# Kernel tuning notes

Measured on AMD Instinct MI355X. Metric: run time of the kernel, lower is better.

The kernel has to match this reference:

```python
import jax, jax.numpy as jnp
import numpy as np

N_NODES = 100000
N_EDGES = 1600000
NUM_FEATURES = 128
HIDDEN = 64
NUM_CLASSES = 2


def _gcn_norm(edge_index, num_nodes):
    # PyG gcn_norm: add self-loops, symmetric degree normalization.
    loop = jnp.arange(num_nodes, dtype=edge_index.dtype)
    src = jnp.concatenate([edge_index[0], loop])
    dst = jnp.concatenate([edge_index[1], loop])
    deg = jax.ops.segment_sum(jnp.ones_like(src, dtype=jnp.float32), dst,
                              num_segments=num_nodes)
    dinv = jnp.where(deg > 0, jax.lax.rsqrt(deg), 0.0)
    norm = dinv[src] * dinv[dst]  # [E + N]
    return src, dst, norm


def _gcn_conv(x, src, dst, norm, W, b, num_nodes):
    h = x @ W  # linear transform first (PyG GCNConv)
    msg = h[src] * norm[:, None]  # gather + edge scaling, [E+N, H]
    out = jax.ops.segment_sum(msg, dst, num_segments=num_nodes)  # scatter-add
    return out + b


def setup_inputs() -> dict:
    key = jax.random.key(0)
    ks = jax.random.split(key, 8)
    x = jax.random.normal(ks[0], (N_NODES, NUM_FEATURES), dtype=jnp.float32)
    edge_index = jax.random.randint(ks[1], (2, N_EDGES), 0, N_NODES, dtype=jnp.int32)
    def glorot(k, shape):
        lim = np.sqrt(6.0 / (shape[0] + shape[1]))
        return jax.random.uniform(k, shape, jnp.float32, -lim, lim)
    return {
        "x": x,
        "edge_index": edge_index,
        "W1": glorot(ks[2], (NUM_FEATURES, HIDDEN)),
        "b1": jnp.zeros((HIDDEN,), jnp.float32),
        "W2": glorot(ks[3], (HIDDEN, HIDDEN)),
        "b2": jnp.zeros((HIDDEN,), jnp.float32),
        "W3": glorot(ks[4], (HIDDEN, HIDDEN)),
        "b3": jnp.zeros((HIDDEN,), jnp.float32),
        "Wlin": glorot(ks[5], (HIDDEN, NUM_CLASSES)),
        "blin": jnp.zeros((NUM_CLASSES,), jnp.float32),
    }


def reference(x, edge_index, W1, b1, W2, b2, W3, b3, Wlin, blin):
    num_nodes = x.shape[0]
    src, dst, norm = _gcn_norm(edge_index, num_nodes)
    # eval mode: dropout is identity
    h = jax.nn.relu(_gcn_conv(x, src, dst, norm, W1, b1, num_nodes))
    h = jax.nn.relu(_gcn_conv(h, src, dst, norm, W2, b2, num_nodes))
    h = jax.nn.relu(_gcn_conv(h, src, dst, norm, W3, b3, num_nodes))
    logits = h @ Wlin + blin
    return jax.nn.log_softmax(logits, axis=1)
```

## Files before the change

kernel.cpp:

```cpp
#include <hip/hip_runtime.h>
#include <cstdint>
#include <cstddef>

#define NF 128
#define NH 64


__global__ __launch_bounds__(256) void count_kernel(const int* __restrict__ ei, int E,
                                                    int* __restrict__ cnt) {
  int i = blockIdx.x * 256 + threadIdx.x;
  if (i * 4 >= E) return;
  int4 d = ((const int4*)(ei + E))[i];
  atomicAdd(&cnt[d.x], 1);
  atomicAdd(&cnt[d.y], 1);
  atomicAdd(&cnt[d.z], 1);
  atomicAdd(&cnt[d.w], 1);
}

__global__ __launch_bounds__(256) void partial_kernel(const int* __restrict__ cnt, int N,
                                                      int* __restrict__ part) {
  __shared__ int sd[256];
  int t = threadIdx.x;
  int idx = blockIdx.x * 1024 + t * 4;
  int s = 0;
#pragma unroll
  for (int j = 0; j < 4; ++j)
    if (idx + j < N) s += cnt[idx + j];
  sd[t] = s;
  __syncthreads();
  for (int off = 128; off > 0; off >>= 1) {
    if (t < off) sd[t] += sd[t + off];
    __syncthreads();
  }
  if (t == 0) part[blockIdx.x] = sd[0];
}

__global__ __launch_bounds__(128) void scanp_kernel(int* __restrict__ part, int NB,
                                                    int* __restrict__ rowptrN) {
  __shared__ int s[128];
  int t = threadIdx.x;
  int v = (t < NB) ? part[t] : 0;
  s[t] = v;
  __syncthreads();
  for (int off = 1; off < 128; off <<= 1) {
    int add = (t >= off) ? s[t - off] : 0;
    __syncthreads();
    s[t] += add;
    __syncthreads();
  }
  if (t < NB) part[t] = s[t] - v;
  if (t == 0) rowptrN[0] = s[127];
}

__global__ __launch_bounds__(256) void rowptr_kernel(const int* __restrict__ cnt,
                                                     const int* __restrict__ part,
                                                     int* __restrict__ rowptr,
                                                     int* __restrict__ cnt2,
                                                     float* __restrict__ dinv, int N) {
  __shared__ int s[256];
  int t = threadIdx.x;
  int idx = blockIdx.x * 1024 + t * 4;
  int c[4];
  int ts = 0;
#pragma unroll
  for (int j = 0; j < 4; ++j) {
    c[j] = (idx + j < N) ? cnt[idx + j] : 0;
    ts += c[j];
  }
  s[t] = ts;
  __syncthreads();
  for (int off = 1; off < 256; off <<= 1) {
    int add = (t >= off) ? s[t - off] : 0;
    __syncthreads();
    s[t] += add;
    __syncthreads();
  }
  int run = s[t] - ts + part[blockIdx.x];
#pragma unroll
  for (int j = 0; j < 4; ++j) {
    if (idx + j < N) {
      rowptr[idx + j] = run;
      cnt2[idx + j] = run;
      dinv[idx + j] = rsqrtf((float)(c[j] + 1));
    }
    run += c[j];
  }
}

__global__ __launch_bounds__(256) void fill_kernel(const int* __restrict__ ei, int E,
                                                   int* __restrict__ cnt2,
                                                   const float* __restrict__ dinv,
                                                   int2* __restrict__ col2,
                                                   int lo, int hi) {
  int i = blockIdx.x * 256 + threadIdx.x;
  if (i * 4 >= E) return;
  int4 sv = ((const int4*)ei)[i];
  int4 dv = ((const int4*)(ei + E))[i];
  int ss[4] = {sv.x, sv.y, sv.z, sv.w};
  int dd[4] = {dv.x, dv.y, dv.z, dv.w};
#pragma unroll
  for (int j = 0; j < 4; ++j) {
    int d = dd[j];
    if (d < lo || d >= hi) continue;
    int s = ss[j];
    float w = dinv[s] * dinv[d];
    int pos = atomicAdd(&cnt2[d], 1);
    col2[pos] = make_int2(s, __float_as_int(w));
  }
}


template <int K>
__global__ __launch_bounds__(256, 4) void gemm_kernel(const float* __restrict__ X,
                                                      const float* __restrict__ W,
                                                      float* __restrict__ H, int N) {
  __shared__ float XsT[64][68];
  __shared__ float Ws[64 * 64];
  const int tid = threadIdx.x;
  const int n0 = blockIdx.x * 64;
  const int tn = (tid >> 4) * 4;
  const int tf = (tid & 15) * 4;

  float acc[4][4];
#pragma unroll
  for (int i = 0; i < 4; ++i)
#pragma unroll
    for (int j = 0; j < 4; ++j) acc[i][j] = 0.f;

  for (int kt = 0; kt < K / 64; ++kt) {
    {
      const float4* Wg = (const float4*)(W + (size_t)kt * 64 * 64);
      float4* Wl = (float4*)Ws;
#pragma unroll
      for (int j = 0; j < 4; ++j) Wl[tid + j * 256] = Wg[tid + j * 256];
    }
#pragma unroll
    for (int j = 0; j < 4; ++j) {
      int idx = tid + j * 256;
      int n = idx >> 4;
      int kq = idx & 15;
      float4 v = make_float4(0.f, 0.f, 0.f, 0.f);
      if (n0 + n < N)
        v = *(const float4*)(X + (size_t)(n0 + n) * K + kt * 64 + kq * 4);
      XsT[kq * 4 + 0][n] = v.x;
      XsT[kq * 4 + 1][n] = v.y;
      XsT[kq * 4 + 2][n] = v.z;
      XsT[kq * 4 + 3][n] = v.w;
    }
    __syncthreads();
#pragma unroll 8
    for (int k = 0; k < 64; ++k) {
      float4 xv = *(const float4*)(&XsT[k][tn]);
      float4 wv = *(const float4*)(&Ws[k * 64 + tf]);
      acc[0][0] = fmaf(xv.x, wv.x, acc[0][0]);
      acc[0][1] = fmaf(xv.x, wv.y, acc[0][1]);
      acc[0][2] = fmaf(xv.x, wv.z, acc[0][2]);
      acc[0][3] = fmaf(xv.x, wv.w, acc[0][3]);
      acc[1][0] = fmaf(xv.y, wv.x, acc[1][0]);
      acc[1][1] = fmaf(xv.y, wv.y, acc[1][1]);
      acc[1][2] = fmaf(xv.y, wv.z, acc[1][2]);
      acc[1][3] = fmaf(xv.y, wv.w, acc[1][3]);
      acc[2][0] = fmaf(xv.z, wv.x, acc[2][0]);
      acc[2][1] = fmaf(xv.z, wv.y, acc[2][1]);
      acc[2][2] = fmaf(xv.z, wv.z, acc[2][2]);
      acc[2][3] = fmaf(xv.z, wv.w, acc[2][3]);
      acc[3][0] = fmaf(xv.w, wv.x, acc[3][0]);
      acc[3][1] = fmaf(xv.w, wv.y, acc[3][1]);
      acc[3][2] = fmaf(xv.w, wv.z, acc[3][2]);
      acc[3][3] = fmaf(xv.w, wv.w, acc[3][3]);
    }
    __syncthreads();
  }
#pragma unroll
  for (int i = 0; i < 4; ++i) {
    int n = n0 + tn + i;
    if (n < N)
      *(float4*)(H + (size_t)n * 64 + tf) =
          make_float4(acc[i][0], acc[i][1], acc[i][2], acc[i][3]);
  }
}

template <int FINAL>
__global__ __launch_bounds__(256, 4) void prop_fused_kernel(
    const float* __restrict__ H, const int* __restrict__ rowptr,
    const int2* __restrict__ col2, const float* __restrict__ dinv,
    const float* __restrict__ bias, const float* __restrict__ Wn,
    const float* __restrict__ blin, float* __restrict__ out, int N) {
  __shared__ float Ws[64 * 64];
  __shared__ float rbuf[4][64];
  const int lane = threadIdx.x & 63;
  const int widx = threadIdx.x >> 6;

  if (!FINAL) {
    const float4* Wg = (const float4*)Wn;
    float4* Wl = (float4*)Ws;
    for (int i = threadIdx.x; i < 1024; i += 256) Wl[i] = Wg[i];
    __syncthreads();
  }

  int n = blockIdx.x * 4 + widx;
  n = __builtin_amdgcn_readfirstlane(n);
  if (n >= N) return;

  float wl0 = 0.f, wl1 = 0.f, bl0 = 0.f, bl1 = 0.f;
  if (FINAL) {
    wl0 = Wn[lane * 2 + 0];
    wl1 = Wn[lane * 2 + 1];
    bl0 = blin[0];
    bl1 = blin[1];
  }

  int e0 = rowptr[n];
  int e1 = rowptr[n + 1];
  float di = dinv[n];
  float acc = H[(size_t)n * 64 + lane] * (di * di);
  int e = e0;
  for (; e + 16 <= e1; e += 16) {
    int2 c[16];
#pragma unroll
    for (int j = 0; j < 16; ++j) c[j] = col2[e + j];
    float h[16];
#pragma unroll
    for (int j = 0; j < 16; ++j) h[j] = H[(size_t)c[j].x * 64 + lane];
#pragma unroll
    for (int j = 0; j < 16; ++j) acc = fmaf(__int_as_float(c[j].y), h[j], acc);
  }
  for (; e + 4 <= e1; e += 4) {
    int2 c[4];
#pragma unroll
    for (int j = 0; j < 4; ++j) c[j] = col2[e + j];
    float h[4];
#pragma unroll
    for (int j = 0; j < 4; ++j) h[j] = H[(size_t)c[j].x * 64 + lane];
#pragma unroll
    for (int j = 0; j < 4; ++j) acc = fmaf(__int_as_float(c[j].y), h[j], acc);
  }
  for (; e < e1; ++e) {
    int2 c = col2[e];
    acc = fmaf(__int_as_float(c.y), H[(size_t)c.x * 64 + lane], acc);
  }
  float r = acc + bias[lane];
  r = r > 0.f ? r : 0.f;

  if (FINAL) {
    float t0 = r * wl0;
    float t1 = r * wl1;
#pragma unroll
    for (int off = 32; off > 0; off >>= 1) {
      t0 += __shfl_xor(t0, off, 64);
      t1 += __shfl_xor(t1, off, 64);
    }
    if (lane == 0) {
      float l0 = t0 + bl0;
      float l1 = t1 + bl1;
      float m = fmaxf(l0, l1);
      float lz = m + logf(expf(l0 - m) + expf(l1 - m));
      out[(size_t)n * 2 + 0] = l0 - lz;
      out[(size_t)n * 2 + 1] = l1 - lz;
    }
  } else {
    rbuf[widx][lane] = r;
    __builtin_amdgcn_wave_barrier();
    float o = 0.f;
#pragma unroll
    for (int q = 0; q < 16; ++q) {
      float4 rv = *(const float4*)(&rbuf[widx][4 * q]);
      o = fmaf(rv.x, Ws[(4 * q + 0) * 64 + lane], o);
      o = fmaf(rv.y, Ws[(4 * q + 1) * 64 + lane], o);
      o = fmaf(rv.z, Ws[(4 * q + 2) * 64 + lane], o);
      o = fmaf(rv.w, Ws[(4 * q + 3) * 64 + lane], o);
    }
    out[(size_t)n * 64 + lane] = o;
  }
}


extern "C" void kernel_launch(void* const* d_in, const int* in_sizes, int n_in,
                              void* d_out, int out_size, void* d_ws, size_t ws_size,
                              hipStream_t stream) {
  const float* x  = (const float*)d_in[0];
  const int*   ei = (const int*)d_in[1];
  const float* W1 = (const float*)d_in[2];
  const float* b1 = (const float*)d_in[3];
  const float* W2 = (const float*)d_in[4];
  const float* b2 = (const float*)d_in[5];
  const float* W3 = (const float*)d_in[6];
  const float* b3 = (const float*)d_in[7];
  const float* Wl = (const float*)d_in[8];
  const float* bl = (const float*)d_in[9];
  float* out = (float*)d_out;

  const int N = in_sizes[0] / NF;
  const int E = in_sizes[1] / 2;

  char* w = (char*)d_ws;
  size_t off = 0;
  auto alloc = [&](size_t bytes) {
    void* p = w + off;
    off += bytes;
    off = (off + 15) & ~(size_t)15;
    return p;
  };
  int*   cnt    = (int*)alloc((size_t)N * 4);
  int*   cnt2   = (int*)alloc((size_t)N * 4);
  int*   rowptr = (int*)alloc((size_t)(N + 1) * 4);
  int*   part   = (int*)alloc(256 * 4);
  float* dinv   = (float*)alloc((size_t)N * 4);
  int2*  col2   = (int2*)alloc((size_t)E * 8);
  float* hA     = (float*)alloc((size_t)N * NH * 4);
  float* hB     = (float*)alloc((size_t)N * NH * 4);

  const int NB = (N + 1023) / 1024;

  hipMemsetAsync(cnt, 0, (size_t)N * 4, stream);
  hipLaunchKernelGGL(count_kernel, dim3((E / 4 + 255) / 256), dim3(256), 0, stream,
                     ei, E, cnt);
  hipLaunchKernelGGL(partial_kernel, dim3(NB), dim3(256), 0, stream, cnt, N, part);
  hipLaunchKernelGGL(scanp_kernel, dim3(1), dim3(128), 0, stream, part, NB, rowptr + N);
  hipLaunchKernelGGL(rowptr_kernel, dim3(NB), dim3(256), 0, stream,
                     cnt, part, rowptr, cnt2, dinv, N);

  const int P = 8;
  const int RW = (N + P - 1) / P;
  for (int p = 0; p < P; ++p) {
    hipLaunchKernelGGL(fill_kernel, dim3((E / 4 + 255) / 256), dim3(256), 0, stream,
                       ei, E, cnt2, dinv, col2, p * RW, (p + 1) * RW);
  }

  hipLaunchKernelGGL(gemm_kernel<128>, dim3((N + 63) / 64), dim3(256), 0, stream, x, W1, hA, N);
  hipLaunchKernelGGL(prop_fused_kernel<0>, dim3((N + 3) / 4), dim3(256), 0, stream,
                     hA, rowptr, col2, dinv, b1, W2, (const float*)nullptr, hB, N);
  hipLaunchKernelGGL(prop_fused_kernel<0>, dim3((N + 3) / 4), dim3(256), 0, stream,
                     hB, rowptr, col2, dinv, b2, W3, (const float*)nullptr, hA, N);
  hipLaunchKernelGGL(prop_fused_kernel<1>, dim3((N + 3) / 4), dim3(256), 0, stream,
                     hA, rowptr, col2, dinv, b3, Wl, bl, out, N);
}
```

Measured before the change: 492.2 us.

## Merge partitioned fill passes into one launch and software-pipeline edge gathers

The eight separate fill_kernel launches become a single launch whose blocks take their destination-range pass from the low bits of the block index. count_kernel gets the same range partitioning so its atomics are grouped by destination range. The propagation kernel drops its 16/4/1 unrolled gather loops for an 8-wide loop that prefetches the next edge batch while the current gathers are in flight, splits the sum across two accumulators, and removes the occupancy hint from launch_bounds. This is meant to cut launch overhead and hide gather latency, at the cost of more registers and an eightfold read of the destination array in count_kernel.

```diff
diff --git a/kernel.cpp b/kernel.cpp
--- a/kernel.cpp
+++ b/kernel.cpp
@@ -7,14 +7,16 @@
 
 
 __global__ __launch_bounds__(256) void count_kernel(const int* __restrict__ ei, int E,
-                                                    int* __restrict__ cnt) {
-  int i = blockIdx.x * 256 + threadIdx.x;
+                                                    int* __restrict__ cnt, int RW) {
+  int pass = blockIdx.x & 7;
+  int i = (blockIdx.x >> 3) * 256 + threadIdx.x;
   if (i * 4 >= E) return;
   int4 d = ((const int4*)(ei + E))[i];
-  atomicAdd(&cnt[d.x], 1);
-  atomicAdd(&cnt[d.y], 1);
-  atomicAdd(&cnt[d.z], 1);
-  atomicAdd(&cnt[d.w], 1);
+  int lo = pass * RW, hi = lo + RW;
+  if (d.x >= lo && d.x < hi) atomicAdd(&cnt[d.x], 1);
+  if (d.y >= lo && d.y < hi) atomicAdd(&cnt[d.y], 1);
+  if (d.z >= lo && d.z < hi) atomicAdd(&cnt[d.z], 1);
+  if (d.w >= lo && d.w < hi) atomicAdd(&cnt[d.w], 1);
 }
 
 __global__ __launch_bounds__(256) void partial_kernel(const int* __restrict__ cnt, int N,
@@ -90,12 +92,13 @@
 __global__ __launch_bounds__(256) void fill_kernel(const int* __restrict__ ei, int E,
                                                    int* __restrict__ cnt2,
                                                    const float* __restrict__ dinv,
-                                                   int2* __restrict__ col2,
-                                                   int lo, int hi) {
-  int i = blockIdx.x * 256 + threadIdx.x;
+                                                   int2* __restrict__ col2, int RW) {
+  int pass = blockIdx.x & 7;
+  int i = (blockIdx.x >> 3) * 256 + threadIdx.x;
   if (i * 4 >= E) return;
   int4 sv = ((const int4*)ei)[i];
   int4 dv = ((const int4*)(ei + E))[i];
+  int lo = pass * RW, hi = lo + RW;
   int ss[4] = {sv.x, sv.y, sv.z, sv.w};
   int dd[4] = {dv.x, dv.y, dv.z, dv.w};
 #pragma unroll
@@ -181,7 +184,7 @@
 }
 
 template <int FINAL>
-__global__ __launch_bounds__(256, 4) void prop_fused_kernel(
+__global__ __launch_bounds__(256) void prop_fused_kernel(
     const float* __restrict__ H, const int* __restrict__ rowptr,
     const int2* __restrict__ col2, const float* __restrict__ dinv,
     const float* __restrict__ bias, const float* __restrict__ Wn,
@@ -213,33 +216,50 @@
   int e0 = rowptr[n];
   int e1 = rowptr[n + 1];
   float di = dinv[n];
-  float acc = H[(size_t)n * 64 + lane] * (di * di);
-  int e = e0;
-  for (; e + 16 <= e1; e += 16) {
-    int2 c[16];
-#pragma unroll
-    for (int j = 0; j < 16; ++j) c[j] = col2[e + j];
-    float h[16];
-#pragma unroll
-    for (int j = 0; j < 16; ++j) h[j] = H[(size_t)c[j].x * 64 + lane];
-#pragma unroll
-    for (int j = 0; j < 16; ++j) acc = fmaf(__int_as_float(c[j].y), h[j], acc);
-  }
-  for (; e + 4 <= e1; e += 4) {
-    int2 c[4];
-#pragma unroll
-    for (int j = 0; j < 4; ++j) c[j] = col2[e + j];
-    float h[4];
-#pragma unroll
-    for (int j = 0; j < 4; ++j) h[j] = H[(size_t)c[j].x * 64 + lane];
-#pragma unroll
-    for (int j = 0; j < 4; ++j) acc = fmaf(__int_as_float(c[j].y), h[j], acc);
-  }
-  for (; e < e1; ++e) {
-    int2 c = col2[e];
-    acc = fmaf(__int_as_float(c.y), H[(size_t)c.x * 64 + lane], acc);
-  }
-  float r = acc + bias[lane];
+  const int2* ec = col2 + e0;
+  const int m = e1 - e0;
+
+  float acc0 = H[(size_t)n * 64 + lane] * (di * di);
+  float acc1 = 0.f;
+
+  int sC[8], sN[8];
+  float wC[8], wN[8];
+  const int nfull = m >> 3;
+
+#define LOADC(S, W, base)                           \
+  {                                                 \
+    _Pragma("unroll") for (int j = 0; j < 8; ++j) { \
+      int2 c = ec[(base) + j];                      \
+      S[j] = c.x;                                   \
+      W[j] = __int_as_float(c.y);                   \
+    }                                               \
+  }
+
+  if (nfull > 0) LOADC(sC, wC, 0)
+  for (int b = 0; b < nfull; ++b) {
+    float h[8];
+#pragma unroll
+    for (int j = 0; j < 8; ++j) h[j] = H[(size_t)sC[j] * 64 + lane];
+    if (b + 1 < nfull) LOADC(sN, wN, (b + 1) * 8)
+#pragma unroll
+    for (int j = 0; j < 8; ++j) {
+      if (j & 1)
+        acc1 = fmaf(wC[j], h[j], acc1);
+      else
+        acc0 = fmaf(wC[j], h[j], acc0);
+    }
+#pragma unroll
+    for (int j = 0; j < 8; ++j) {
+      sC[j] = sN[j];
+      wC[j] = wN[j];
+    }
+  }
+#undef LOADC
+  for (int t = nfull * 8; t < m; ++t) {
+    int2 c = ec[t];
+    acc0 = fmaf(__int_as_float(c.y), H[(size_t)c.x * 64 + lane], acc0);
+  }
+  float r = acc0 + acc1 + bias[lane];
   r = r > 0.f ? r : 0.f;
 
   if (FINAL) {
@@ -253,8 +273,8 @@
     if (lane == 0) {
       float l0 = t0 + bl0;
       float l1 = t1 + bl1;
-      float m = fmaxf(l0, l1);
-      float lz = m + logf(expf(l0 - m) + expf(l1 - m));
+      float mx = fmaxf(l0, l1);
+      float lz = mx + logf(expf(l0 - mx) + expf(l1 - mx));
       out[(size_t)n * 2 + 0] = l0 - lz;
       out[(size_t)n * 2 + 1] = l1 - lz;
     }
@@ -311,21 +331,18 @@
   float* hB     = (float*)alloc((size_t)N * NH * 4);
 
   const int NB = (N + 1023) / 1024;
+  const int RW = (N + 7) / 8;
+  const int NCHUNK = (E / 4 + 255) / 256;
 
   hipMemsetAsync(cnt, 0, (size_t)N * 4, stream);
-  hipLaunchKernelGGL(count_kernel, dim3((E / 4 + 255) / 256), dim3(256), 0, stream,
-                     ei, E, cnt);
+  hipLaunchKernelGGL(count_kernel, dim3(8 * NCHUNK), dim3(256), 0, stream,
+                     ei, E, cnt, RW);
   hipLaunchKernelGGL(partial_kernel, dim3(NB), dim3(256), 0, stream, cnt, N, part);
   hipLaunchKernelGGL(scanp_kernel, dim3(1), dim3(128), 0, stream, part, NB, rowptr + N);
   hipLaunchKernelGGL(rowptr_kernel, dim3(NB), dim3(256), 0, stream,
                      cnt, part, rowptr, cnt2, dinv, N);
-
-  const int P = 8;
-  const int RW = (N + P - 1) / P;
-  for (int p = 0; p < P; ++p) {
-    hipLaunchKernelGGL(fill_kernel, dim3((E / 4 + 255) / 256), dim3(256), 0, stream,
-                       ei, E, cnt2, dinv, col2, p * RW, (p + 1) * RW);
-  }
+  hipLaunchKernelGGL(fill_kernel, dim3(8 * NCHUNK), dim3(256), 0, stream,
+                     ei, E, cnt2, dinv, col2, RW);
 
   hipLaunchKernelGGL(gemm_kernel<128>, dim3((N + 63) / 64), dim3(256), 0, stream, x, W1, hA, N);
   hipLaunchKernelGGL(prop_fused_kernel<0>, dim3((N + 3) / 4), dim3(256), 0, stream,
```

Measured after the change: 459.8 us. 1.07x faster.
